# Kernel tuning notes

Measured on AMD Instinct MI355X. Metric: run time of the kernel, lower is better.

## Reference

```python
import jax, jax.numpy as jnp
import numpy as np

G, NPG, HC, LAT, FF, EDIM, EH = 8, 4096, 16, 64, 512, 3, 64
N = G * NPG            # 32768 total nodes
E = 393216             # avg degree 12


def setup_inputs() -> dict:
    key = jax.random.key(0)
    ks = jax.random.split(key, 16)
    w = lambda k, s: jax.random.normal(k, s, jnp.float32) * 0.02
    inp = {
        "x": jax.random.normal(ks[0], (G, LAT), jnp.float32),
        "edge_index": jax.random.randint(ks[1], (2, E), 0, N, dtype=jnp.int64),
        "edge_attr": jax.random.normal(ks[2], (E, EDIM), jnp.float32),
        "fc2_w": w(ks[3], (LAT, FF)),   "fc2_b": jnp.zeros((FF,), jnp.float32),
        "fc1_w": w(ks[4], (FF, NPG * HC)), "fc1_b": jnp.zeros((NPG * HC,), jnp.float32),
    }
    for i in range(2):
        inp[f"conv{i}_root"] = w(ks[5 + 4 * i], (HC, HC))
        inp[f"conv{i}_bias"] = jnp.zeros((HC,), jnp.float32)
        inp[f"conv{i}_w1"] = w(ks[6 + 4 * i], (EDIM, EH))
        inp[f"conv{i}_b1"] = jnp.zeros((EH,), jnp.float32)
        inp[f"conv{i}_w2"] = w(ks[7 + 4 * i], (EH, HC * HC))
        inp[f"conv{i}_b2"] = jnp.zeros((HC * HC,), jnp.float32)
    return inp


def _nnconv(x, src, dst, ea, root, bias, w1, b1, w2, b2):
    # edge-conditioned conv (NNConv): per-edge weight matrix from edge MLP
    theta = (jax.nn.relu(ea @ w1 + b1) @ w2 + b2).reshape(-1, HC, HC)  # [E,HC,HC]
    msg = jnp.einsum('ei,eio->eo', x[src], theta)                       # gather+per-edge matvec
    aggr = jax.ops.segment_sum(msg, dst, num_segments=N)                # scatter-add
    return x @ root + aggr + bias


def reference(x, edge_index, edge_attr, fc2_w, fc2_b, fc1_w, fc1_b,
              conv0_root, conv0_bias, conv0_w1, conv0_b1, conv0_w2, conv0_b2,
              conv1_root, conv1_bias, conv1_w1, conv1_b1, conv1_w2, conv1_b2):
    h = x @ fc2_w + fc2_b                      # [G, FF]
    h = jax.nn.elu(h @ fc1_w + fc1_b)          # [G, NPG*HC]
    h = h.reshape(N, HC)                       # node features
    src, dst = edge_index[0], edge_index[1]
    convs = ((conv0_root, conv0_bias, conv0_w1, conv0_b1, conv0_w2, conv0_b2),
             (conv1_root, conv1_bias, conv1_w1, conv1_b1, conv1_w2, conv1_b2))
    for (root, b, w1, b1, w2, b2) in convs:
        h = jax.nn.elu(_nnconv(h, src, dst, edge_attr, root, b, w1, b1, w2, b2))
        # dropout is identity in eval mode
    return h
```

## Files before the change

kernel.cpp:

```cpp
#include <hip/hip_runtime.h>
#include <math.h>

#define G_   8
#define NPG_ 4096
#define HC_  16
#define LAT_ 64
#define FF_  512
#define EDIM_ 3
#define EH_  64
#define NN_  32768
#define EE_  393216

__global__ void k_front1(const float* __restrict__ x, const float* __restrict__ w,
                         const float* __restrict__ b, float* __restrict__ h1) {
  int c = blockIdx.x * blockDim.x + threadIdx.x;
  if (c >= FF_) return;
  float acc[G_];
#pragma unroll
  for (int g = 0; g < G_; g++) acc[g] = 0.f;
  for (int r = 0; r < LAT_; r++) {
    float wv = w[r * FF_ + c];
#pragma unroll
    for (int g = 0; g < G_; g++) acc[g] = fmaf(x[g * LAT_ + r], wv, acc[g]);
  }
#pragma unroll
  for (int g = 0; g < G_; g++) h1[g * FF_ + c] = acc[g] + b[c];
}

__global__ __launch_bounds__(512) void k_front2(const float* __restrict__ h1,
                                                const float* __restrict__ w,
                                                const float* __restrict__ b,
                                                float* __restrict__ hn) {
  __shared__ float sh[G_ * FF_];
  for (int i = threadIdx.x; i < G_ * FF_; i += blockDim.x) sh[i] = h1[i];
  __syncthreads();
  int g = threadIdx.x >> 6;
  int lane = threadIdx.x & 63;
  int c = blockIdx.x * 64 + lane;
  const float* shg = &sh[g * FF_];
  float acc = 0.f;
#pragma unroll 8
  for (int r = 0; r < FF_; r++) acc = fmaf(shg[r], w[r * (NPG_ * HC_) + c], acc);
  float v = acc + b[c];
  hn[g * (NPG_ * HC_) + c] = v > 0.f ? v : expm1f(v);
}

__global__ void k_zero(int* __restrict__ p, int nv) {
  int i = blockIdx.x * blockDim.x + threadIdx.x;
  if (i < nv) p[i] = 0;
}
__global__ void k_hist(const int* __restrict__ key, int* __restrict__ cnt) {
  int e = blockIdx.x * blockDim.x + threadIdx.x;
  if (e < EE_) atomicAdd(&cnt[key[e]], 1);
}
__global__ __launch_bounds__(1024) void k_scan(const int* __restrict__ cnt,
                                               int* __restrict__ rowptr,
                                               int* __restrict__ cursor) {
  __shared__ int part[1024];
  int t = threadIdx.x;
  int base = t * 32;
  int loc[32];
  int s = 0;
#pragma unroll
  for (int i = 0; i < 32; i++) { loc[i] = s; s += cnt[base + i]; }
  part[t] = s;
  __syncthreads();
  for (int off = 1; off < 1024; off <<= 1) {
    int v = (t >= off) ? part[t - off] : 0;
    __syncthreads();
    part[t] += v;
    __syncthreads();
  }
  int pre = (t == 0) ? 0 : part[t - 1];
#pragma unroll
  for (int i = 0; i < 32; i++) {
    int v = pre + loc[i];
    rowptr[base + i] = v;
    cursor[base + i] = v;
  }
  if (t == 1023) rowptr[NN_] = part[1023];
}
__global__ void k_scatter(const int* __restrict__ src, const int* __restrict__ dst,
                          const float* __restrict__ ea, int* __restrict__ cursor,
                          float4* __restrict__ eas4) {
  int e = blockIdx.x * blockDim.x + threadIdx.x;
  if (e < EE_) {
    int pos = atomicAdd(&cursor[src[e]], 1);
    eas4[pos] = make_float4(ea[e * 3], ea[e * 3 + 1], ea[e * 3 + 2],
                            __int_as_float(dst[e]));
  } else if (e < EE_ + 8) {
    eas4[e] = make_float4(0.f, 0.f, 0.f, __int_as_float(0));
  }
}

__global__ void k_nodeinit(const float* __restrict__ hn, const float* __restrict__ root,
                           const float* __restrict__ bias, float* __restrict__ out) {
  int idx = blockIdx.x * blockDim.x + threadIdx.x;
  if (idx >= NN_ * HC_) return;
  int nd = idx >> 4, o = idx & 15;
  float acc = bias[o];
#pragma unroll
  for (int i = 0; i < 16; i++) acc = fmaf(hn[nd * 16 + i], root[i * 16 + o], acc);
  out[idx] = acc;
}

__global__ void k_wprep(const float* __restrict__ w2, const float* __restrict__ w1,
                        const float* __restrict__ b1, float* __restrict__ W2m,
                        float4* __restrict__ w1p4) {
  int idx = blockIdx.x * 256 + threadIdx.x;
  if (idx < 16384) {
    int i  = idx >> 10;
    int j4 = (idx >> 8) & 3;
    int l  = (idx >> 2) & 63;
    int c  = idx & 3;
    int q = l >> 4, o = l & 15;
    int h = q * 16 + j4 * 4 + c;
    W2m[idx] = w2[h * 256 + i * 16 + o];
  }
  if (idx < 64) {
    w1p4[idx] = make_float4(w1[idx], w1[64 + idx], w1[128 + idx], b1[idx]);
  }
}

__global__ __launch_bounds__(256, 4) void k_precM(
    const float* __restrict__ hn, const float* __restrict__ W2m,
    float4* __restrict__ Mbuf4) {
  int tid = threadIdx.x;
  int wave = tid >> 6, l = tid & 63;
  int n0 = (blockIdx.x * 4 + wave) * 4;
  const float4* __restrict__ W2m4 = (const float4*)W2m;

  float4 a0[4], a1[4], a2[4], a3[4];
#pragma unroll
  for (int j4 = 0; j4 < 4; j4++) {
    a0[j4] = make_float4(0.f, 0.f, 0.f, 0.f);
    a1[j4] = make_float4(0.f, 0.f, 0.f, 0.f);
    a2[j4] = make_float4(0.f, 0.f, 0.f, 0.f);
    a3[j4] = make_float4(0.f, 0.f, 0.f, 0.f);
  }
  for (int i = 0; i < 16; i++) {
    float x0 = hn[(n0 + 0) * 16 + i];
    float x1 = hn[(n0 + 1) * 16 + i];
    float x2 = hn[(n0 + 2) * 16 + i];
    float x3 = hn[(n0 + 3) * 16 + i];
#pragma unroll
    for (int j4 = 0; j4 < 4; j4++) {
      float4 w = W2m4[i * 256 + j4 * 64 + l];
      a0[j4].x = fmaf(x0, w.x, a0[j4].x); a0[j4].y = fmaf(x0, w.y, a0[j4].y);
      a0[j4].z = fmaf(x0, w.z, a0[j4].z); a0[j4].w = fmaf(x0, w.w, a0[j4].w);
      a1[j4].x = fmaf(x1, w.x, a1[j4].x); a1[j4].y = fmaf(x1, w.y, a1[j4].y);
      a1[j4].z = fmaf(x1, w.z, a1[j4].z); a1[j4].w = fmaf(x1, w.w, a1[j4].w);
      a2[j4].x = fmaf(x2, w.x, a2[j4].x); a2[j4].y = fmaf(x2, w.y, a2[j4].y);
      a2[j4].z = fmaf(x2, w.z, a2[j4].z); a2[j4].w = fmaf(x2, w.w, a2[j4].w);
      a3[j4].x = fmaf(x3, w.x, a3[j4].x); a3[j4].y = fmaf(x3, w.y, a3[j4].y);
      a3[j4].z = fmaf(x3, w.z, a3[j4].z); a3[j4].w = fmaf(x3, w.w, a3[j4].w);
    }
  }
  int s0 = n0 * 256;
#pragma unroll
  for (int j4 = 0; j4 < 4; j4++) Mbuf4[s0 + j4 * 64 + l] = a0[j4];
#pragma unroll
  for (int j4 = 0; j4 < 4; j4++) Mbuf4[s0 + 256 + j4 * 64 + l] = a1[j4];
#pragma unroll
  for (int j4 = 0; j4 < 4; j4++) Mbuf4[s0 + 512 + j4 * 64 + l] = a2[j4];
#pragma unroll
  for (int j4 = 0; j4 < 4; j4++) Mbuf4[s0 + 768 + j4 * 64 + l] = a3[j4];
}

__global__ __launch_bounds__(256, 4) void k_edge(
    const float* __restrict__ hn, const int* __restrict__ rowptr,
    const float4* __restrict__ eas4, const float4* __restrict__ w1p4,
    const float* __restrict__ b2, const float4* __restrict__ Mbuf4,
    float* __restrict__ hnext) {
  __shared__ float4 sw1[64];
  int tid = threadIdx.x;
  if (tid < 64) sw1[tid] = w1p4[tid];
  __syncthreads();

  int wave = tid >> 6, l = tid & 63;
  int o = l & 15, q = l >> 4;
  int n = blockIdx.x * 4 + wave;

  int rs = rowptr[n], re = rowptr[n + 1];
  if (rs >= re) return;

  int mb = n * 256 + l;
  float4 m0 = Mbuf4[mb], m1 = Mbuf4[mb + 64], m2 = Mbuf4[mb + 128],
         m3 = Mbuf4[mb + 192];
  float M[16] = {m0.x, m0.y, m0.z, m0.w, m1.x, m1.y, m1.z, m1.w,
                 m2.x, m2.y, m2.z, m2.w, m3.x, m3.y, m3.z, m3.w};

  const float4* __restrict__ hx4 = (const float4*)&hn[n * 16];
  float T = 0.f;
#pragma unroll
  for (int i4 = 0; i4 < 4; i4++) {
    float4 xq = hx4[i4];
    T = fmaf(xq.x, b2[(i4 * 4 + 0) * 16 + o], T);
    T = fmaf(xq.y, b2[(i4 * 4 + 1) * 16 + o], T);
    T = fmaf(xq.z, b2[(i4 * 4 + 2) * 16 + o], T);
    T = fmaf(xq.w, b2[(i4 * 4 + 3) * 16 + o], T);
  }

  const float4* __restrict__ w1v = &sw1[q * 16];

  float4 c0 = eas4[rs], c1 = eas4[rs + 1], c2 = eas4[rs + 2], c3 = eas4[rs + 3];
  for (int k = rs; k < re; k += 4) {
    float4 n0 = eas4[k + 4], n1 = eas4[k + 5], n2 = eas4[k + 6], n3 = eas4[k + 7];

    float p0 = 0.f, p1 = 0.f, p2 = 0.f, p3 = 0.f;
#pragma unroll
    for (int j = 0; j < 16; j++) {
      float4 wv = w1v[j];
      float m = M[j];
      float h0 = fmaxf(fmaf(c0.z, wv.z, fmaf(c0.y, wv.y, fmaf(c0.x, wv.x, wv.w))), 0.f);
      float h1 = fmaxf(fmaf(c1.z, wv.z, fmaf(c1.y, wv.y, fmaf(c1.x, wv.x, wv.w))), 0.f);
      float h2 = fmaxf(fmaf(c2.z, wv.z, fmaf(c2.y, wv.y, fmaf(c2.x, wv.x, wv.w))), 0.f);
      float h3 = fmaxf(fmaf(c3.z, wv.z, fmaf(c3.y, wv.y, fmaf(c3.x, wv.x, wv.w))), 0.f);
      p0 = fmaf(h0, m, p0);
      p1 = fmaf(h1, m, p1);
      p2 = fmaf(h2, m, p2);
      p3 = fmaf(h3, m, p3);
    }
    p0 += __shfl_xor(p0, 16); p1 += __shfl_xor(p1, 16);
    p2 += __shfl_xor(p2, 16); p3 += __shfl_xor(p3, 16);
    p0 += __shfl_xor(p0, 32); p1 += __shfl_xor(p1, 32);
    p2 += __shfl_xor(p2, 32); p3 += __shfl_xor(p3, 32);

    float vv  = (q == 0) ? p0   : (q == 1) ? p1   : (q == 2) ? p2   : p3;
    float dpf = (q == 0) ? c0.w : (q == 1) ? c1.w : (q == 2) ? c2.w : c3.w;
    if (k + q < re) atomicAdd(&hnext[__float_as_int(dpf) * 16 + o], vv + T);

    c0 = n0; c1 = n1; c2 = n2; c3 = n3;
  }
}

__global__ void k_elu(const float* __restrict__ in, float* __restrict__ out) {
  int idx = blockIdx.x * blockDim.x + threadIdx.x;
  if (idx >= NN_ * HC_) return;
  float v = in[idx];
  out[idx] = v > 0.f ? v : expm1f(v);
}

extern "C" void kernel_launch(void* const* d_in, const int* in_sizes, int n_in,
                              void* d_out, int out_size, void* d_ws, size_t ws_size,
                              hipStream_t stream) {
  const float* x    = (const float*)d_in[0];
  const int*   ei   = (const int*)d_in[1];
  const float* ea   = (const float*)d_in[2];
  const float* fc2w = (const float*)d_in[3];
  const float* fc2b = (const float*)d_in[4];
  const float* fc1w = (const float*)d_in[5];
  const float* fc1b = (const float*)d_in[6];
  float* out = (float*)d_out;

  float* ws = (float*)d_ws;
  float*  h1     = ws;
  float*  hnode  = h1 + 4096;
  float*  hnext  = hnode + (size_t)NN_ * HC_;
  float*  W2m    = hnext + (size_t)NN_ * HC_;
  float4* w1p4   = (float4*)(W2m + 16384);
  float4* eas4   = (float4*)((float*)w1p4 + 256);
  float4* Mbuf4  = (float4*)((float*)eas4 + (size_t)(EE_ + 8) * 4);
  int*    cnt    = (int*)((float*)Mbuf4 + (size_t)NN_ * 1024);
  int*    rowptr = cnt + NN_;
  int*    cursor = rowptr + NN_ + 1;

  const int* src  = ei;
  const int* dstp = ei + EE_;

  k_front1<<<2, 256, 0, stream>>>(x, fc2w, fc2b, h1);
  k_front2<<<1024, 512, 0, stream>>>(h1, fc1w, fc1b, hnode);

  k_zero<<<(NN_ + 255) / 256, 256, 0, stream>>>(cnt, NN_);
  k_hist<<<(EE_ + 255) / 256, 256, 0, stream>>>(src, cnt);
  k_scan<<<1, 1024, 0, stream>>>(cnt, rowptr, cursor);
  k_scatter<<<(EE_ + 8 + 255) / 256, 256, 0, stream>>>(src, dstp, ea, cursor, eas4);

  for (int cv = 0; cv < 2; cv++) {
    const float* root = (const float*)d_in[7 + cv * 6];
    const float* cb   = (const float*)d_in[8 + cv * 6];
    const float* w1   = (const float*)d_in[9 + cv * 6];
    const float* b1   = (const float*)d_in[10 + cv * 6];
    const float* w2   = (const float*)d_in[11 + cv * 6];
    const float* b2   = (const float*)d_in[12 + cv * 6];
    k_wprep<<<64, 256, 0, stream>>>(w2, w1, b1, W2m, w1p4);
    k_nodeinit<<<NN_ * HC_ / 256, 256, 0, stream>>>(hnode, root, cb, hnext);
    k_precM<<<NN_ / 16, 256, 0, stream>>>(hnode, W2m, Mbuf4);
    k_edge<<<NN_ / 4, 256, 0, stream>>>(hnode, rowptr, eas4, w1p4, b2, Mbuf4, hnext);
    k_elu<<<NN_ * HC_ / 256, 256, 0, stream>>>(hnext, cv == 0 ? hnode : out);
  }
}
```

Measured before the change: 365.4 us.

## Switch edge kernel to one thread per edge with precomputed bias term

```diff
diff --git a/kernel.cpp b/kernel.cpp
--- a/kernel.cpp
+++ b/kernel.cpp
@@ -82,15 +82,14 @@
 }
 __global__ void k_scatter(const int* __restrict__ src, const int* __restrict__ dst,
                           const float* __restrict__ ea, int* __restrict__ cursor,
-                          float4* __restrict__ eas4) {
+                          float4* __restrict__ eas4, int* __restrict__ srcn) {
   int e = blockIdx.x * blockDim.x + threadIdx.x;
-  if (e < EE_) {
-    int pos = atomicAdd(&cursor[src[e]], 1);
-    eas4[pos] = make_float4(ea[e * 3], ea[e * 3 + 1], ea[e * 3 + 2],
-                            __int_as_float(dst[e]));
-  } else if (e < EE_ + 8) {
-    eas4[e] = make_float4(0.f, 0.f, 0.f, __int_as_float(0));
-  }
+  if (e >= EE_) return;
+  int sn = src[e];
+  int pos = atomicAdd(&cursor[sn], 1);
+  eas4[pos] = make_float4(ea[e * 3], ea[e * 3 + 1], ea[e * 3 + 2],
+                          __int_as_float(dst[e]));
+  srcn[pos] = sn;
 }
 
 __global__ void k_nodeinit(const float* __restrict__ hn, const float* __restrict__ root,
@@ -109,12 +108,9 @@
                         float4* __restrict__ w1p4) {
   int idx = blockIdx.x * 256 + threadIdx.x;
   if (idx < 16384) {
-    int i  = idx >> 10;
-    int j4 = (idx >> 8) & 3;
-    int l  = (idx >> 2) & 63;
-    int c  = idx & 3;
-    int q = l >> 4, o = l & 15;
-    int h = q * 16 + j4 * 4 + c;
+    int i = idx >> 10;
+    int h = (idx >> 4) & 63;
+    int o = idx & 15;
     W2m[idx] = w2[h * 256 + i * 16 + o];
   }
   if (idx < 64) {
@@ -124,114 +120,96 @@
 
 __global__ __launch_bounds__(256, 4) void k_precM(
     const float* __restrict__ hn, const float* __restrict__ W2m,
-    float4* __restrict__ Mbuf4) {
+    const float* __restrict__ b2, float4* __restrict__ Mbuf4,
+    float* __restrict__ Tbuf) {
   int tid = threadIdx.x;
   int wave = tid >> 6, l = tid & 63;
-  int n0 = (blockIdx.x * 4 + wave) * 4;
+  int n0 = (blockIdx.x * 4 + wave) * 2;
   const float4* __restrict__ W2m4 = (const float4*)W2m;
 
-  float4 a0[4], a1[4], a2[4], a3[4];
-#pragma unroll
-  for (int j4 = 0; j4 < 4; j4++) {
-    a0[j4] = make_float4(0.f, 0.f, 0.f, 0.f);
-    a1[j4] = make_float4(0.f, 0.f, 0.f, 0.f);
-    a2[j4] = make_float4(0.f, 0.f, 0.f, 0.f);
-    a3[j4] = make_float4(0.f, 0.f, 0.f, 0.f);
-  }
+  float4 A0 = {0,0,0,0}, A1 = {0,0,0,0}, A2 = {0,0,0,0}, A3 = {0,0,0,0};
+  float4 B0 = {0,0,0,0}, B1 = {0,0,0,0}, B2 = {0,0,0,0}, B3 = {0,0,0,0};
   for (int i = 0; i < 16; i++) {
-    float x0 = hn[(n0 + 0) * 16 + i];
-    float x1 = hn[(n0 + 1) * 16 + i];
-    float x2 = hn[(n0 + 2) * 16 + i];
-    float x3 = hn[(n0 + 3) * 16 + i];
-#pragma unroll
-    for (int j4 = 0; j4 < 4; j4++) {
-      float4 w = W2m4[i * 256 + j4 * 64 + l];
-      a0[j4].x = fmaf(x0, w.x, a0[j4].x); a0[j4].y = fmaf(x0, w.y, a0[j4].y);
-      a0[j4].z = fmaf(x0, w.z, a0[j4].z); a0[j4].w = fmaf(x0, w.w, a0[j4].w);
-      a1[j4].x = fmaf(x1, w.x, a1[j4].x); a1[j4].y = fmaf(x1, w.y, a1[j4].y);
-      a1[j4].z = fmaf(x1, w.z, a1[j4].z); a1[j4].w = fmaf(x1, w.w, a1[j4].w);
-      a2[j4].x = fmaf(x2, w.x, a2[j4].x); a2[j4].y = fmaf(x2, w.y, a2[j4].y);
-      a2[j4].z = fmaf(x2, w.z, a2[j4].z); a2[j4].w = fmaf(x2, w.w, a2[j4].w);
-      a3[j4].x = fmaf(x3, w.x, a3[j4].x); a3[j4].y = fmaf(x3, w.y, a3[j4].y);
-      a3[j4].z = fmaf(x3, w.z, a3[j4].z); a3[j4].w = fmaf(x3, w.w, a3[j4].w);
-    }
-  }
-  int s0 = n0 * 256;
-#pragma unroll
-  for (int j4 = 0; j4 < 4; j4++) Mbuf4[s0 + j4 * 64 + l] = a0[j4];
-#pragma unroll
-  for (int j4 = 0; j4 < 4; j4++) Mbuf4[s0 + 256 + j4 * 64 + l] = a1[j4];
-#pragma unroll
-  for (int j4 = 0; j4 < 4; j4++) Mbuf4[s0 + 512 + j4 * 64 + l] = a2[j4];
-#pragma unroll
-  for (int j4 = 0; j4 < 4; j4++) Mbuf4[s0 + 768 + j4 * 64 + l] = a3[j4];
+    float xA = hn[n0 * 16 + i];
+    float xB = hn[n0 * 16 + 16 + i];
+    float4 w0 = W2m4[i * 256 + l * 4 + 0];
+    float4 w1v = W2m4[i * 256 + l * 4 + 1];
+    float4 w2v = W2m4[i * 256 + l * 4 + 2];
+    float4 w3v = W2m4[i * 256 + l * 4 + 3];
+    A0.x = fmaf(xA, w0.x, A0.x); A0.y = fmaf(xA, w0.y, A0.y);
+    A0.z = fmaf(xA, w0.z, A0.z); A0.w = fmaf(xA, w0.w, A0.w);
+    A1.x = fmaf(xA, w1v.x, A1.x); A1.y = fmaf(xA, w1v.y, A1.y);
+    A1.z = fmaf(xA, w1v.z, A1.z); A1.w = fmaf(xA, w1v.w, A1.w);
+    A2.x = fmaf(xA, w2v.x, A2.x); A2.y = fmaf(xA, w2v.y, A2.y);
+    A2.z = fmaf(xA, w2v.z, A2.z); A2.w = fmaf(xA, w2v.w, A2.w);
+    A3.x = fmaf(xA, w3v.x, A3.x); A3.y = fmaf(xA, w3v.y, A3.y);
+    A3.z = fmaf(xA, w3v.z, A3.z); A3.w = fmaf(xA, w3v.w, A3.w);
+    B0.x = fmaf(xB, w0.x, B0.x); B0.y = fmaf(xB, w0.y, B0.y);
+    B0.z = fmaf(xB, w0.z, B0.z); B0.w = fmaf(xB, w0.w, B0.w);
+    B1.x = fmaf(xB, w1v.x, B1.x); B1.y = fmaf(xB, w1v.y, B1.y);
+    B1.z = fmaf(xB, w1v.z, B1.z); B1.w = fmaf(xB, w1v.w, B1.w);
+    B2.x = fmaf(xB, w2v.x, B2.x); B2.y = fmaf(xB, w2v.y, B2.y);
+    B2.z = fmaf(xB, w2v.z, B2.z); B2.w = fmaf(xB, w2v.w, B2.w);
+    B3.x = fmaf(xB, w3v.x, B3.x); B3.y = fmaf(xB, w3v.y, B3.y);
+    B3.z = fmaf(xB, w3v.z, B3.z); B3.w = fmaf(xB, w3v.w, B3.w);
+  }
+  int s0 = n0 * 256 + l * 4;
+  Mbuf4[s0 + 0] = A0; Mbuf4[s0 + 1] = A1; Mbuf4[s0 + 2] = A2; Mbuf4[s0 + 3] = A3;
+  Mbuf4[s0 + 256 + 0] = B0; Mbuf4[s0 + 256 + 1] = B1;
+  Mbuf4[s0 + 256 + 2] = B2; Mbuf4[s0 + 256 + 3] = B3;
+
+  if (l < 32) {
+    int nn = n0 + (l >> 4);
+    int o = l & 15;
+    float t = 0.f;
+#pragma unroll
+    for (int i = 0; i < 16; i++) t = fmaf(hn[nn * 16 + i], b2[i * 16 + o], t);
+    Tbuf[nn * 16 + o] = t;
+  }
 }
 
 __global__ __launch_bounds__(256, 4) void k_edge(
-    const float* __restrict__ hn, const int* __restrict__ rowptr,
-    const float4* __restrict__ eas4, const float4* __restrict__ w1p4,
-    const float* __restrict__ b2, const float4* __restrict__ Mbuf4,
-    float* __restrict__ hnext) {
-  __shared__ float4 sw1[64];
+    const int* __restrict__ srcn, const float4* __restrict__ eas4,
+    const float4* __restrict__ w1p4, const float4* __restrict__ Mbuf4,
+    const float4* __restrict__ Tbuf4, float* __restrict__ hnext) {
   int tid = threadIdx.x;
-  if (tid < 64) sw1[tid] = w1p4[tid];
-  __syncthreads();
-
-  int wave = tid >> 6, l = tid & 63;
-  int o = l & 15, q = l >> 4;
-  int n = blockIdx.x * 4 + wave;
-
-  int rs = rowptr[n], re = rowptr[n + 1];
-  if (rs >= re) return;
-
-  int mb = n * 256 + l;
-  float4 m0 = Mbuf4[mb], m1 = Mbuf4[mb + 64], m2 = Mbuf4[mb + 128],
-         m3 = Mbuf4[mb + 192];
-  float M[16] = {m0.x, m0.y, m0.z, m0.w, m1.x, m1.y, m1.z, m1.w,
-                 m2.x, m2.y, m2.z, m2.w, m3.x, m3.y, m3.z, m3.w};
-
-  const float4* __restrict__ hx4 = (const float4*)&hn[n * 16];
-  float T = 0.f;
-#pragma unroll
-  for (int i4 = 0; i4 < 4; i4++) {
-    float4 xq = hx4[i4];
-    T = fmaf(xq.x, b2[(i4 * 4 + 0) * 16 + o], T);
-    T = fmaf(xq.y, b2[(i4 * 4 + 1) * 16 + o], T);
-    T = fmaf(xq.z, b2[(i4 * 4 + 2) * 16 + o], T);
-    T = fmaf(xq.w, b2[(i4 * 4 + 3) * 16 + o], T);
-  }
-
-  const float4* __restrict__ w1v = &sw1[q * 16];
-
-  float4 c0 = eas4[rs], c1 = eas4[rs + 1], c2 = eas4[rs + 2], c3 = eas4[rs + 3];
-  for (int k = rs; k < re; k += 4) {
-    float4 n0 = eas4[k + 4], n1 = eas4[k + 5], n2 = eas4[k + 6], n3 = eas4[k + 7];
-
-    float p0 = 0.f, p1 = 0.f, p2 = 0.f, p3 = 0.f;
-#pragma unroll
-    for (int j = 0; j < 16; j++) {
-      float4 wv = w1v[j];
-      float m = M[j];
-      float h0 = fmaxf(fmaf(c0.z, wv.z, fmaf(c0.y, wv.y, fmaf(c0.x, wv.x, wv.w))), 0.f);
-      float h1 = fmaxf(fmaf(c1.z, wv.z, fmaf(c1.y, wv.y, fmaf(c1.x, wv.x, wv.w))), 0.f);
-      float h2 = fmaxf(fmaf(c2.z, wv.z, fmaf(c2.y, wv.y, fmaf(c2.x, wv.x, wv.w))), 0.f);
-      float h3 = fmaxf(fmaf(c3.z, wv.z, fmaf(c3.y, wv.y, fmaf(c3.x, wv.x, wv.w))), 0.f);
-      p0 = fmaf(h0, m, p0);
-      p1 = fmaf(h1, m, p1);
-      p2 = fmaf(h2, m, p2);
-      p3 = fmaf(h3, m, p3);
-    }
-    p0 += __shfl_xor(p0, 16); p1 += __shfl_xor(p1, 16);
-    p2 += __shfl_xor(p2, 16); p3 += __shfl_xor(p3, 16);
-    p0 += __shfl_xor(p0, 32); p1 += __shfl_xor(p1, 32);
-    p2 += __shfl_xor(p2, 32); p3 += __shfl_xor(p3, 32);
-
-    float vv  = (q == 0) ? p0   : (q == 1) ? p1   : (q == 2) ? p2   : p3;
-    float dpf = (q == 0) ? c0.w : (q == 1) ? c1.w : (q == 2) ? c2.w : c3.w;
-    if (k + q < re) atomicAdd(&hnext[__float_as_int(dpf) * 16 + o], vv + T);
-
-    c0 = n0; c1 = n1; c2 = n2; c3 = n3;
-  }
+  int e = (blockIdx.x * 4 + (tid >> 6)) * 64 + (tid & 63);
+
+  float4 ea = eas4[e];
+  int ni = srcn[e];
+  int d = __float_as_int(ea.w);
+  const float4* __restrict__ Mb = &Mbuf4[ni * 256];
+  const float4* __restrict__ Tb = &Tbuf4[ni * 4];
+  float4 p0 = Tb[0], p1 = Tb[1], p2 = Tb[2], p3 = Tb[3];
+
+#pragma unroll 2
+  for (int h = 0; h < 64; h++) {
+    float4 wv = w1p4[h];
+    float hd = fmaf(ea.z, wv.z, fmaf(ea.y, wv.y, fmaf(ea.x, wv.x, wv.w)));
+    hd = fmaxf(hd, 0.f);
+    float4 m0 = Mb[h * 4 + 0];
+    float4 m1 = Mb[h * 4 + 1];
+    float4 m2 = Mb[h * 4 + 2];
+    float4 m3 = Mb[h * 4 + 3];
+    p0.x = fmaf(hd, m0.x, p0.x); p0.y = fmaf(hd, m0.y, p0.y);
+    p0.z = fmaf(hd, m0.z, p0.z); p0.w = fmaf(hd, m0.w, p0.w);
+    p1.x = fmaf(hd, m1.x, p1.x); p1.y = fmaf(hd, m1.y, p1.y);
+    p1.z = fmaf(hd, m1.z, p1.z); p1.w = fmaf(hd, m1.w, p1.w);
+    p2.x = fmaf(hd, m2.x, p2.x); p2.y = fmaf(hd, m2.y, p2.y);
+    p2.z = fmaf(hd, m2.z, p2.z); p2.w = fmaf(hd, m2.w, p2.w);
+    p3.x = fmaf(hd, m3.x, p3.x); p3.y = fmaf(hd, m3.y, p3.y);
+    p3.z = fmaf(hd, m3.z, p3.z); p3.w = fmaf(hd, m3.w, p3.w);
+  }
+
+  float* __restrict__ row = &hnext[d * 16];
+  atomicAdd(row + 0,  p0.x); atomicAdd(row + 1,  p0.y);
+  atomicAdd(row + 2,  p0.z); atomicAdd(row + 3,  p0.w);
+  atomicAdd(row + 4,  p1.x); atomicAdd(row + 5,  p1.y);
+  atomicAdd(row + 6,  p1.z); atomicAdd(row + 7,  p1.w);
+  atomicAdd(row + 8,  p2.x); atomicAdd(row + 9,  p2.y);
+  atomicAdd(row + 10, p2.z); atomicAdd(row + 11, p2.w);
+  atomicAdd(row + 12, p3.x); atomicAdd(row + 13, p3.y);
+  atomicAdd(row + 14, p3.z); atomicAdd(row + 15, p3.w);
 }
 
 __global__ void k_elu(const float* __restrict__ in, float* __restrict__ out) {
@@ -261,7 +239,9 @@
   float4* w1p4   = (float4*)(W2m + 16384);
   float4* eas4   = (float4*)((float*)w1p4 + 256);
   float4* Mbuf4  = (float4*)((float*)eas4 + (size_t)(EE_ + 8) * 4);
-  int*    cnt    = (int*)((float*)Mbuf4 + (size_t)NN_ * 1024);
+  float*  Tbuf   = (float*)Mbuf4 + (size_t)NN_ * 1024;
+  int*    srcn   = (int*)(Tbuf + (size_t)NN_ * HC_);
+  int*    cnt    = srcn + EE_;
   int*    rowptr = cnt + NN_;
   int*    cursor = rowptr + NN_ + 1;
 
@@ -274,7 +254,8 @@
   k_zero<<<(NN_ + 255) / 256, 256, 0, stream>>>(cnt, NN_);
   k_hist<<<(EE_ + 255) / 256, 256, 0, stream>>>(src, cnt);
   k_scan<<<1, 1024, 0, stream>>>(cnt, rowptr, cursor);
-  k_scatter<<<(EE_ + 8 + 255) / 256, 256, 0, stream>>>(src, dstp, ea, cursor, eas4);
+  k_scatter<<<(EE_ + 255) / 256, 256, 0, stream>>>(src, dstp, ea, cursor,
+                                                   eas4, srcn);
 
   for (int cv = 0; cv < 2; cv++) {
     const float* root = (const float*)d_in[7 + cv * 6];
@@ -285,8 +266,9 @@
     const float* b2   = (const float*)d_in[12 + cv * 6];
     k_wprep<<<64, 256, 0, stream>>>(w2, w1, b1, W2m, w1p4);
     k_nodeinit<<<NN_ * HC_ / 256, 256, 0, stream>>>(hnode, root, cb, hnext);
-    k_precM<<<NN_ / 16, 256, 0, stream>>>(hnode, W2m, Mbuf4);
-    k_edge<<<NN_ / 4, 256, 0, stream>>>(hnode, rowptr, eas4, w1p4, b2, Mbuf4, hnext);
+    k_precM<<<NN_ / 8, 256, 0, stream>>>(hnode, W2m, b2, Mbuf4, Tbuf);
+    k_edge<<<EE_ / 256, 256, 0, stream>>>(srcn, eas4, w1p4, Mbuf4,
+                                          (const float4*)Tbuf, hnext);
     k_elu<<<NN_ * HC_ / 256, 256, 0, stream>>>(hnext, cv == 0 ? hnode : out);
   }
 }
```

Measured after the change: 1.069 ms. 2.93x slower.

## Fuse node init, ELU and M precompute; degree-sort nodes for edge kernel

Applied to the files above, without the earlier changes.

```diff
diff --git a/kernel.cpp b/kernel.cpp
--- a/kernel.cpp
+++ b/kernel.cpp
@@ -93,15 +93,30 @@
   }
 }
 
-__global__ void k_nodeinit(const float* __restrict__ hn, const float* __restrict__ root,
-                           const float* __restrict__ bias, float* __restrict__ out) {
-  int idx = blockIdx.x * blockDim.x + threadIdx.x;
-  if (idx >= NN_ * HC_) return;
-  int nd = idx >> 4, o = idx & 15;
-  float acc = bias[o];
-#pragma unroll
-  for (int i = 0; i < 16; i++) acc = fmaf(hn[nd * 16 + i], root[i * 16 + o], acc);
-  out[idx] = acc;
+__global__ void k_dhist(const int* __restrict__ cnt, int* __restrict__ dcnt) {
+  int n = blockIdx.x * blockDim.x + threadIdx.x;
+  if (n < NN_) {
+    int d = cnt[n]; if (d > 255) d = 255;
+    atomicAdd(&dcnt[255 - d], 1);
+  }
+}
+__global__ void k_dscan(const int* __restrict__ dcnt, int* __restrict__ dcur) {
+  __shared__ int tmp[256];
+  int t = threadIdx.x;
+  tmp[t] = dcnt[t];
+  __syncthreads();
+  int acc = 0;
+  for (int i = 0; i < t; i++) acc += tmp[i];
+  dcur[t] = acc;
+}
+__global__ void k_dscatter(const int* __restrict__ cnt, int* __restrict__ dcur,
+                           int* __restrict__ norder) {
+  int n = blockIdx.x * blockDim.x + threadIdx.x;
+  if (n < NN_) {
+    int d = cnt[n]; if (d > 255) d = 255;
+    int pos = atomicAdd(&dcur[255 - d], 1);
+    norder[pos] = n;
+  }
 }
 
 __global__ void k_wprep(const float* __restrict__ w2, const float* __restrict__ w1,
@@ -122,14 +137,32 @@
   }
 }
 
-__global__ __launch_bounds__(256, 4) void k_precM(
-    const float* __restrict__ hn, const float* __restrict__ W2m,
-    float4* __restrict__ Mbuf4) {
+__global__ __launch_bounds__(256, 4) void k_node(
+    const float* __restrict__ hin, const int do_elu,
+    const float* __restrict__ root, const float* __restrict__ bias,
+    const float* __restrict__ W2m, float* __restrict__ hnode,
+    float* __restrict__ hnext, float4* __restrict__ Mbuf4) {
+  __shared__ float sx[256];
   int tid = threadIdx.x;
   int wave = tid >> 6, l = tid & 63;
   int n0 = (blockIdx.x * 4 + wave) * 4;
+  float* swx = &sx[wave * 64];
+
+  float v = hin[n0 * 16 + l];
+  if (do_elu) {
+    v = v > 0.f ? v : expm1f(v);
+    hnode[n0 * 16 + l] = v;
+  }
+  swx[l] = v;
+
+  int nd = l >> 4, o = l & 15;
+  float acc = bias[o];
+#pragma unroll
+  for (int i = 0; i < 16; i++)
+    acc = fmaf(swx[nd * 16 + i], root[i * 16 + o], acc);
+  hnext[(n0 + nd) * 16 + o] = acc;
+
   const float4* __restrict__ W2m4 = (const float4*)W2m;
-
   float4 a0[4], a1[4], a2[4], a3[4];
 #pragma unroll
   for (int j4 = 0; j4 < 4; j4++) {
@@ -139,10 +172,10 @@
     a3[j4] = make_float4(0.f, 0.f, 0.f, 0.f);
   }
   for (int i = 0; i < 16; i++) {
-    float x0 = hn[(n0 + 0) * 16 + i];
-    float x1 = hn[(n0 + 1) * 16 + i];
-    float x2 = hn[(n0 + 2) * 16 + i];
-    float x3 = hn[(n0 + 3) * 16 + i];
+    float x0 = swx[i];
+    float x1 = swx[16 + i];
+    float x2 = swx[32 + i];
+    float x3 = swx[48 + i];
 #pragma unroll
     for (int j4 = 0; j4 < 4; j4++) {
       float4 w = W2m4[i * 256 + j4 * 64 + l];
@@ -171,15 +204,15 @@
     const float* __restrict__ hn, const int* __restrict__ rowptr,
     const float4* __restrict__ eas4, const float4* __restrict__ w1p4,
     const float* __restrict__ b2, const float4* __restrict__ Mbuf4,
-    float* __restrict__ hnext) {
-  __shared__ float4 sw1[64];
+    float* __restrict__ hnext, const int* __restrict__ norder) {
+  __shared__ float4 sw1[4 * 17];
   int tid = threadIdx.x;
-  if (tid < 64) sw1[tid] = w1p4[tid];
+  if (tid < 64) sw1[(tid >> 4) * 17 + (tid & 15)] = w1p4[tid];
   __syncthreads();
 
   int wave = tid >> 6, l = tid & 63;
   int o = l & 15, q = l >> 4;
-  int n = blockIdx.x * 4 + wave;
+  int n = norder[blockIdx.x * 4 + wave];
 
   int rs = rowptr[n], re = rowptr[n + 1];
   if (rs >= re) return;
@@ -201,7 +234,7 @@
     T = fmaf(xq.w, b2[(i4 * 4 + 3) * 16 + o], T);
   }
 
-  const float4* __restrict__ w1v = &sw1[q * 16];
+  const float4* __restrict__ w1v = &sw1[q * 17];
 
   float4 c0 = eas4[rs], c1 = eas4[rs + 1], c2 = eas4[rs + 2], c3 = eas4[rs + 3];
   for (int k = rs; k < re; k += 4) {
@@ -264,6 +297,9 @@
   int*    cnt    = (int*)((float*)Mbuf4 + (size_t)NN_ * 1024);
   int*    rowptr = cnt + NN_;
   int*    cursor = rowptr + NN_ + 1;
+  int*    norder = cursor + NN_;
+  int*    dcnt   = norder + NN_;
+  int*    dcur   = dcnt + 256;
 
   const int* src  = ei;
   const int* dstp = ei + EE_;
@@ -275,6 +311,10 @@
   k_hist<<<(EE_ + 255) / 256, 256, 0, stream>>>(src, cnt);
   k_scan<<<1, 1024, 0, stream>>>(cnt, rowptr, cursor);
   k_scatter<<<(EE_ + 8 + 255) / 256, 256, 0, stream>>>(src, dstp, ea, cursor, eas4);
+  k_zero<<<1, 256, 0, stream>>>(dcnt, 256);
+  k_dhist<<<NN_ / 256, 256, 0, stream>>>(cnt, dcnt);
+  k_dscan<<<1, 256, 0, stream>>>(dcnt, dcur);
+  k_dscatter<<<NN_ / 256, 256, 0, stream>>>(cnt, dcur, norder);
 
   for (int cv = 0; cv < 2; cv++) {
     const float* root = (const float*)d_in[7 + cv * 6];
@@ -284,9 +324,10 @@
     const float* w2   = (const float*)d_in[11 + cv * 6];
     const float* b2   = (const float*)d_in[12 + cv * 6];
     k_wprep<<<64, 256, 0, stream>>>(w2, w1, b1, W2m, w1p4);
-    k_nodeinit<<<NN_ * HC_ / 256, 256, 0, stream>>>(hnode, root, cb, hnext);
-    k_precM<<<NN_ / 16, 256, 0, stream>>>(hnode, W2m, Mbuf4);
-    k_edge<<<NN_ / 4, 256, 0, stream>>>(hnode, rowptr, eas4, w1p4, b2, Mbuf4, hnext);
-    k_elu<<<NN_ * HC_ / 256, 256, 0, stream>>>(hnext, cv == 0 ? hnode : out);
-  }
-}
+    k_node<<<NN_ / 16, 256, 0, stream>>>(cv == 0 ? hnode : hnext, cv,
+                                         root, cb, W2m, hnode, hnext, Mbuf4);
+    k_edge<<<NN_ / 4, 256, 0, stream>>>(hnode, rowptr, eas4, w1p4, b2, Mbuf4,
+                                        hnext, norder);
+  }
+  k_elu<<<NN_ * HC_ / 256, 256, 0, stream>>>(hnext, out);
+}
```

New measurement: 547.5 us. +49.8%, slower.
